# Optimization experiments

Hardware: AMD Instinct MI355X
Metric: run time of the kernel (lower is better)

Reference implementation:

```python
import jax, jax.numpy as jnp
import numpy as np


def conv1x1(x, w, b):
    # x: [B,C,H,W], w: [O,C], b: [O] -> [B,O,H,W]
    return jnp.einsum('bchw,oc->bohw', x, w) + b[None, :, None, None]


def setup_inputs() -> dict:
    key = jax.random.key(0)
    ks = jax.random.split(key, 8)
    B, H, W = 32, 64, 64
    PoI_N, PT_feat, T_feat = 128, 64, 32
    poi = jax.random.uniform(ks[0], (B, PoI_N, H, W), dtype=jnp.float32)
    time = jax.random.normal(ks[1], (B, 31, H, W), dtype=jnp.float32)
    s = 0.05
    wm = jax.random.normal(ks[2], (T_feat, 31), dtype=jnp.float32) * s
    bm = jnp.zeros((T_feat,), jnp.float32)
    wf = jax.random.normal(ks[3], (1, T_feat), dtype=jnp.float32) * s
    bf = jnp.zeros((1,), jnp.float32)
    wc = jax.random.normal(ks[4], (PT_feat, PoI_N), dtype=jnp.float32) * s
    bc = jnp.zeros((PT_feat,), jnp.float32)
    return {'poi': poi, 'time': time, 'wm': wm, 'bm': bm, 'wf': wf, 'bf': bf, 'wc': wc, 'bc': bc}


def reference(poi, time, wm, bm, wf, bf, wc, bc):
    # Time_trans: conv1x1 -> relu -> conv1x1 -> relu, out channels = 1
    z = jax.nn.relu(conv1x1(time, wm, bm))
    T_x = jax.nn.relu(conv1x1(z, wf, bf))  # [B,1,H,W]
    # original does a detached CPU tile/multiply: broadcast multiply, no grad through it
    poi_time = jax.lax.stop_gradient(T_x * poi)  # [B,PoI_N,H,W]
    return conv1x1(poi_time, wc, bc)
```

## Files before the change

### kernel.cpp

```cpp
#include <hip/hip_runtime.h>
#include <hip/hip_bf16.h>

typedef short bf16x8 __attribute__((ext_vector_type(8)));
typedef float f32x4  __attribute__((ext_vector_type(4)));

constexpr int HW = 4096;
constexpr int CT = 31;
constexpr int CP = 128;
constexpr int CO = 64;

__device__ __forceinline__ short f2bf(float x) {
    __hip_bfloat16 h = __float2bfloat16(x);
    return *reinterpret_cast<short*>(&h);
}

__global__ __launch_bounds__(256)
void poi_mfma3(const float* __restrict__ poi,
               const float* __restrict__ tin,
               const float* __restrict__ wm,
               const float* __restrict__ bm,
               const float* __restrict__ wf,
               const float* __restrict__ bf,
               const float* __restrict__ wc,
               const float* __restrict__ bc,
               float* __restrict__ out)
{
    const int lane = threadIdx.x & 63;
    const int m    = lane & 15;
    const int g    = lane >> 4;
    const int wid  = threadIdx.x >> 6;
    const int b    = blockIdx.x >> 5;
    const int px0  = ((blockIdx.x & 31) << 7) + wid * 32;

    bf16x8 wcf[4][4];
    #pragma unroll
    for (int s = 0; s < 4; ++s)
      #pragma unroll
      for (int kf = 0; kf < 4; ++kf)
        #pragma unroll
        for (int j = 0; j < 8; ++j)
          wcf[s][kf][j] = f2bf(wc[(s * 16 + m) * CP + kf * 32 + g * 8 + j]);

    bf16x8 wmf[2];
    #pragma unroll
    for (int t2 = 0; t2 < 2; ++t2)
      #pragma unroll
      for (int j = 0; j < 8; ++j) {
        const int c = g * 8 + j;
        wmf[t2][j] = (c < CT) ? f2bf(wm[(t2 * 16 + m) * CT + c]) : (short)0;
      }

    float wff[8]; f32x4 bmf[2]; float bcf[4];
    #pragma unroll
    for (int t2 = 0; t2 < 2; ++t2)
      #pragma unroll
      for (int r = 0; r < 4; ++r) {
        wff[t2 * 4 + r] = wf[t2 * 16 + g * 4 + r];
        bmf[t2][r]      = bm[t2 * 16 + g * 4 + r];
      }
    #pragma unroll
    for (int s = 0; s < 4; ++s) bcf[s] = bc[s * 16 + m];
    const float bfv = bf[0];

    const float* tbase = tin + (size_t)b * CT * HW;
    const float* pbase = poi + (size_t)b * CP * HW;
    float*       obase = out + (size_t)b * CO * HW;

    #pragma unroll
    for (int t = 0; t < 2; ++t) {
        const int pxt = px0 + t * 16;

        const float* tb = tbase + pxt + m;
        bf16x8 tf;
        #pragma unroll
        for (int j = 0; j < 8; ++j) {
            const int c = g * 8 + j;
            tf[j] = (c < CT) ? f2bf(tb[(size_t)c * HW]) : (short)0;
        }
        f32x4 z0 = __builtin_amdgcn_mfma_f32_16x16x32_bf16(wmf[0], tf, bmf[0], 0, 0, 0);
        f32x4 z1 = __builtin_amdgcn_mfma_f32_16x16x32_bf16(wmf[1], tf, bmf[1], 0, 0, 0);
        float s1 = 0.f;
        #pragma unroll
        for (int r = 0; r < 4; ++r) {
            s1 = fmaf(fmaxf(z0[r], 0.f), wff[r],     s1);
            s1 = fmaf(fmaxf(z1[r], 0.f), wff[4 + r], s1);
        }
        s1 += __shfl_xor(s1, 16, 64);
        s1 += __shfl_xor(s1, 32, 64);
        const float tval = fmaxf(s1 + bfv, 0.f);
        f32x4 tv;
        #pragma unroll
        for (int r = 0; r < 4; ++r) tv[r] = __shfl(tval, g * 4 + r, 64);

        const float* pb = pbase + pxt + m;
        bf16x8 pf[4];
        #pragma unroll
        for (int kf = 0; kf < 4; ++kf)
          #pragma unroll
          for (int j = 0; j < 8; ++j)
            pf[kf][j] = f2bf(pb[(size_t)(kf * 32 + g * 8 + j) * HW]);

        float* ob = obase + pxt + g * 4;
        #pragma unroll
        for (int s = 0; s < 4; ++s) {
            f32x4 a = {0.f, 0.f, 0.f, 0.f};
            #pragma unroll
            for (int kf = 0; kf < 4; ++kf)
                a = __builtin_amdgcn_mfma_f32_16x16x32_bf16(pf[kf], wcf[s][kf], a, 0, 0, 0);
            f32x4 v;
            #pragma unroll
            for (int r = 0; r < 4; ++r) v[r] = fmaf(tv[r], a[r], bcf[s]);
            __builtin_nontemporal_store(
                v, reinterpret_cast<f32x4*>(ob + (size_t)(s * 16 + m) * HW));
        }
    }
}

extern "C" void kernel_launch(void* const* d_in, const int* in_sizes, int n_in,
                              void* d_out, int out_size, void* d_ws, size_t ws_size,
                              hipStream_t stream) {
    const float* poi = (const float*)d_in[0];
    const float* tin = (const float*)d_in[1];
    const float* wm  = (const float*)d_in[2];
    const float* bm  = (const float*)d_in[3];
    const float* wf  = (const float*)d_in[4];
    const float* bf  = (const float*)d_in[5];
    const float* wc  = (const float*)d_in[6];
    const float* bc  = (const float*)d_in[7];
    float* out = (float*)d_out;

    hipLaunchKernelGGL(poi_mfma3, dim3(1024), dim3(256), 0, stream,
                       poi, tin, wm, bm, wf, bf, wc, bc, out);
}
```

Baseline: 36.95 us.

## Stage conv weights in LDS as bf16 and hoist all global loads

Each block now converts the 64x128 weight matrix to bf16 once, stores it in shared memory, and reads MFMA B-fragments from LDS instead of holding 64 packed registers per lane. The time and poi loads are issued together up front, behind a scheduling barrier, so more memory requests are in flight before the MFMA chain. A launch-bounds occupancy hint of 4 is added. This trades register pressure for LDS traffic and an extra block-wide barrier, and the 32 float staging registers may offset part of the register savings.

```diff
diff --git a/kernel.cpp b/kernel.cpp
--- a/kernel.cpp
+++ b/kernel.cpp
@@ -13,9 +13,13 @@
     __hip_bfloat16 h = __float2bfloat16(x);
     return *reinterpret_cast<short*>(&h);
 }
+__device__ __forceinline__ unsigned int f2bfu(float x) {
+    __hip_bfloat16 h = __float2bfloat16(x);
+    return (unsigned int)*reinterpret_cast<unsigned short*>(&h);
+}
 
-__global__ __launch_bounds__(256)
-void poi_mfma3(const float* __restrict__ poi,
+__global__ __launch_bounds__(256, 4)
+void poi_mfma4(const float* __restrict__ poi,
                const float* __restrict__ tin,
                const float* __restrict__ wm,
                const float* __restrict__ bm,
@@ -25,21 +29,26 @@
                const float* __restrict__ bc,
                float* __restrict__ out)
 {
-    const int lane = threadIdx.x & 63;
+    __shared__ __align__(16) unsigned short s_wc[CO * CP];
+
+    const int tid  = threadIdx.x;
+    const int lane = tid & 63;
     const int m    = lane & 15;
     const int g    = lane >> 4;
-    const int wid  = threadIdx.x >> 6;
+    const int wid  = tid >> 6;
     const int b    = blockIdx.x >> 5;
     const int px0  = ((blockIdx.x & 31) << 7) + wid * 32;
 
-    bf16x8 wcf[4][4];
-    #pragma unroll
-    for (int s = 0; s < 4; ++s)
-      #pragma unroll
-      for (int kf = 0; kf < 4; ++kf)
+    {
+        unsigned int* d = reinterpret_cast<unsigned int*>(s_wc);
+        const float2* s = reinterpret_cast<const float2*>(wc);
         #pragma unroll
-        for (int j = 0; j < 8; ++j)
-          wcf[s][kf][j] = f2bf(wc[(s * 16 + m) * CP + kf * 32 + g * 8 + j]);
+        for (int i = 0; i < (CO * CP / 2) / 256; ++i) {
+            const int idx = i * 256 + tid;
+            const float2 w2 = s[idx];
+            d[idx] = f2bfu(w2.x) | (f2bfu(w2.y) << 16);
+        }
+    }
 
     bf16x8 wmf[2];
     #pragma unroll
@@ -49,7 +58,6 @@
         const int c = g * 8 + j;
         wmf[t2][j] = (c < CT) ? f2bf(wm[(t2 * 16 + m) * CT + c]) : (short)0;
       }
-
     float wff[8]; f32x4 bmf[2]; float bcf[4];
     #pragma unroll
     for (int t2 = 0; t2 < 2; ++t2)
@@ -62,6 +70,8 @@
     for (int s = 0; s < 4; ++s) bcf[s] = bc[s * 16 + m];
     const float bfv = bf[0];
 
+    __syncthreads();
+
     const float* tbase = tin + (size_t)b * CT * HW;
     const float* pbase = poi + (size_t)b * CP * HW;
     float*       obase = out + (size_t)b * CO * HW;
@@ -69,14 +79,26 @@
     #pragma unroll
     for (int t = 0; t < 2; ++t) {
         const int pxt = px0 + t * 16;
+        const float* tb = tbase + pxt + m;
+        const float* pb = pbase + pxt + m;
 
-        const float* tb = tbase + pxt + m;
-        bf16x8 tf;
+        float tfr[8];
         #pragma unroll
         for (int j = 0; j < 8; ++j) {
             const int c = g * 8 + j;
-            tf[j] = (c < CT) ? f2bf(tb[(size_t)c * HW]) : (short)0;
+            tfr[j] = (c < CT) ? tb[(size_t)c * HW] : 0.f;
         }
+        float pfr[32];
+        #pragma unroll
+        for (int kf = 0; kf < 4; ++kf)
+          #pragma unroll
+          for (int j = 0; j < 8; ++j)
+            pfr[kf * 8 + j] = pb[(size_t)(kf * 32 + g * 8 + j) * HW];
+        __builtin_amdgcn_sched_barrier(0);
+
+        bf16x8 tf;
+        #pragma unroll
+        for (int j = 0; j < 8; ++j) tf[j] = f2bf(tfr[j]);
         f32x4 z0 = __builtin_amdgcn_mfma_f32_16x16x32_bf16(wmf[0], tf, bmf[0], 0, 0, 0);
         f32x4 z1 = __builtin_amdgcn_mfma_f32_16x16x32_bf16(wmf[1], tf, bmf[1], 0, 0, 0);
         float s1 = 0.f;
@@ -92,21 +114,23 @@
         #pragma unroll
         for (int r = 0; r < 4; ++r) tv[r] = __shfl(tval, g * 4 + r, 64);
 
-        const float* pb = pbase + pxt + m;
-        bf16x8 pf[4];
+        bf16x8 pfv[4];
         #pragma unroll
         for (int kf = 0; kf < 4; ++kf)
           #pragma unroll
           for (int j = 0; j < 8; ++j)
-            pf[kf][j] = f2bf(pb[(size_t)(kf * 32 + g * 8 + j) * HW]);
+            pfv[kf][j] = f2bf(pfr[kf * 8 + j]);
 
         float* ob = obase + pxt + g * 4;
         #pragma unroll
         for (int s = 0; s < 4; ++s) {
             f32x4 a = {0.f, 0.f, 0.f, 0.f};
             #pragma unroll
-            for (int kf = 0; kf < 4; ++kf)
-                a = __builtin_amdgcn_mfma_f32_16x16x32_bf16(pf[kf], wcf[s][kf], a, 0, 0, 0);
+            for (int kf = 0; kf < 4; ++kf) {
+                const bf16x8 wv = *reinterpret_cast<const bf16x8*>(
+                    &s_wc[(s * 16 + m) * CP + kf * 32 + g * 8]);
+                a = __builtin_amdgcn_mfma_f32_16x16x32_bf16(pfv[kf], wv, a, 0, 0, 0);
+            }
             f32x4 v;
             #pragma unroll
             for (int r = 0; r < 4; ++r) v[r] = fmaf(tv[r], a[r], bcf[s]);
@@ -129,6 +153,6 @@
     const float* bc  = (const float*)d_in[7];
     float* out = (float*)d_out;
 
-    hipLaunchKernelGGL(poi_mfma3, dim3(1024), dim3(256), 0, stream,
+    hipLaunchKernelGGL(poi_mfma4, dim3(1024), dim3(256), 0, stream,
                        poi, tin, wm, bm, wf, bf, wc, bc, out);
 }
```

After: 54.19 us. 1.47x slower.

## Split output channels across wave pairs and hoist all global loads ahead of compute

Applied to the files above, without the earlier changes.

Each block now covers 64 pixels instead of 128, with pairs of waves splitting the 64 output channels so each wave computes 32. The grid doubles to 2048 blocks and per-wave weight registers shrink. All time and poi loads for a tile are issued first into float registers, with a sched_barrier before conversion and the MFMAs, so the memory loads overlap better. The cost is that each pixel's poi and time data is now read by two waves, and the time-branch MFMAs are computed twice.

```diff
diff --git a/kernel.cpp b/kernel.cpp
--- a/kernel.cpp
+++ b/kernel.cpp
@@ -15,7 +15,7 @@
 }
 
 __global__ __launch_bounds__(256)
-void poi_mfma3(const float* __restrict__ poi,
+void poi_mfma5(const float* __restrict__ poi,
                const float* __restrict__ tin,
                const float* __restrict__ wm,
                const float* __restrict__ bm,
@@ -29,17 +29,18 @@
     const int m    = lane & 15;
     const int g    = lane >> 4;
     const int wid  = threadIdx.x >> 6;
-    const int b    = blockIdx.x >> 5;
-    const int px0  = ((blockIdx.x & 31) << 7) + wid * 32;
+    const int oh   = (wid & 1) * 2;
+    const int b    = blockIdx.x >> 6;
+    const int px0  = ((blockIdx.x & 63) << 6) + (wid >> 1) * 32;
 
-    bf16x8 wcf[4][4];
+    bf16x8 wcf[2][4];
     #pragma unroll
-    for (int s = 0; s < 4; ++s)
+    for (int s = 0; s < 2; ++s)
       #pragma unroll
       for (int kf = 0; kf < 4; ++kf)
         #pragma unroll
         for (int j = 0; j < 8; ++j)
-          wcf[s][kf][j] = f2bf(wc[(s * 16 + m) * CP + kf * 32 + g * 8 + j]);
+          wcf[s][kf][j] = f2bf(wc[((oh + s) * 16 + m) * CP + kf * 32 + g * 8 + j]);
 
     bf16x8 wmf[2];
     #pragma unroll
@@ -49,8 +50,7 @@
         const int c = g * 8 + j;
         wmf[t2][j] = (c < CT) ? f2bf(wm[(t2 * 16 + m) * CT + c]) : (short)0;
       }
-
-    float wff[8]; f32x4 bmf[2]; float bcf[4];
+    float wff[8]; f32x4 bmf[2]; float bcf[2];
     #pragma unroll
     for (int t2 = 0; t2 < 2; ++t2)
       #pragma unroll
@@ -59,7 +59,7 @@
         bmf[t2][r]      = bm[t2 * 16 + g * 4 + r];
       }
     #pragma unroll
-    for (int s = 0; s < 4; ++s) bcf[s] = bc[s * 16 + m];
+    for (int s = 0; s < 2; ++s) bcf[s] = bc[(oh + s) * 16 + m];
     const float bfv = bf[0];
 
     const float* tbase = tin + (size_t)b * CT * HW;
@@ -69,14 +69,26 @@
     #pragma unroll
     for (int t = 0; t < 2; ++t) {
         const int pxt = px0 + t * 16;
+        const float* tb = tbase + pxt + m;
+        const float* pb = pbase + pxt + m;
 
-        const float* tb = tbase + pxt + m;
-        bf16x8 tf;
+        float tfr[8];
         #pragma unroll
         for (int j = 0; j < 8; ++j) {
             const int c = g * 8 + j;
-            tf[j] = (c < CT) ? f2bf(tb[(size_t)c * HW]) : (short)0;
+            tfr[j] = (c < CT) ? tb[(size_t)c * HW] : 0.f;
         }
+        float pfr[32];
+        #pragma unroll
+        for (int kf = 0; kf < 4; ++kf)
+          #pragma unroll
+          for (int j = 0; j < 8; ++j)
+            pfr[kf * 8 + j] = pb[(size_t)(kf * 32 + g * 8 + j) * HW];
+        __builtin_amdgcn_sched_barrier(0);
+
+        bf16x8 tf;
+        #pragma unroll
+        for (int j = 0; j < 8; ++j) tf[j] = f2bf(tfr[j]);
         f32x4 z0 = __builtin_amdgcn_mfma_f32_16x16x32_bf16(wmf[0], tf, bmf[0], 0, 0, 0);
         f32x4 z1 = __builtin_amdgcn_mfma_f32_16x16x32_bf16(wmf[1], tf, bmf[1], 0, 0, 0);
         float s1 = 0.f;
@@ -92,26 +104,25 @@
         #pragma unroll
         for (int r = 0; r < 4; ++r) tv[r] = __shfl(tval, g * 4 + r, 64);
 
-        const float* pb = pbase + pxt + m;
-        bf16x8 pf[4];
+        bf16x8 pfv[4];
         #pragma unroll
         for (int kf = 0; kf < 4; ++kf)
           #pragma unroll
           for (int j = 0; j < 8; ++j)
-            pf[kf][j] = f2bf(pb[(size_t)(kf * 32 + g * 8 + j) * HW]);
+            pfv[kf][j] = f2bf(pfr[kf * 8 + j]);
 
         float* ob = obase + pxt + g * 4;
         #pragma unroll
-        for (int s = 0; s < 4; ++s) {
+        for (int s = 0; s < 2; ++s) {
             f32x4 a = {0.f, 0.f, 0.f, 0.f};
             #pragma unroll
             for (int kf = 0; kf < 4; ++kf)
-                a = __builtin_amdgcn_mfma_f32_16x16x32_bf16(pf[kf], wcf[s][kf], a, 0, 0, 0);
+                a = __builtin_amdgcn_mfma_f32_16x16x32_bf16(pfv[kf], wcf[s][kf], a, 0, 0, 0);
             f32x4 v;
             #pragma unroll
             for (int r = 0; r < 4; ++r) v[r] = fmaf(tv[r], a[r], bcf[s]);
             __builtin_nontemporal_store(
-                v, reinterpret_cast<f32x4*>(ob + (size_t)(s * 16 + m) * HW));
+                v, reinterpret_cast<f32x4*>(ob + (size_t)((oh + s) * 16 + m) * HW));
         }
     }
 }
@@ -129,6 +140,6 @@
     const float* bc  = (const float*)d_in[7];
     float* out = (float*)d_out;
 
-    hipLaunchKernelGGL(poi_mfma3, dim3(1024), dim3(256), 0, stream,
+    hipLaunchKernelGGL(poi_mfma5, dim3(2048), dim3(256), 0, stream,
                        poi, tin, wm, bm, wf, bf, wc, bc, out);
 }
```

Measured after the change: 38.71 us. 1.05x slower.
